# Kernel tuning notes

Measured on AMD Instinct MI355X. Metric: run time of the kernel, lower is better.

Reference implementation:

```python
import jax, jax.numpy as jnp
import numpy as np

B, H, W_, D, K = 64, 28, 28, 512, 32


def setup_inputs() -> dict:
    key = jax.random.key(0)
    k1, k2, k3 = jax.random.split(key, 3)
    x = jax.random.normal(k1, (B, H, W_, D), dtype=jnp.float32)
    # 1x1 conv weight, no bias: [D_in, K] (he_normal-like scale)
    W = jax.random.normal(k2, (D, K), dtype=jnp.float32) * np.sqrt(2.0 / D)
    # cluster offset tensor C (original shape (1,1,1,512,32), squeezed to [D,K])
    C = jax.random.normal(k3, (D, K), dtype=jnp.float32) * np.sqrt(2.0 / D)
    return {"x": x, "W": W, "C": C}


def reference(x, W, C):
    # 1x1 conv == per-pixel matmul: [B,H,W,D] @ [D,K] -> [B,H,W,K]
    s = jnp.einsum('bhwd,dk->bhwk', x, W)
    a = jax.nn.softmax(s, axis=-1)  # soft cluster assignment
    # Original math: v[b,d,k] = sum_{h,w} a[b,h,w,k] * (x[b,h,w,d] + C[d,k])
    # Algebraically identical split avoids the [B,H,W,D,K] 5D intermediate:
    #   sum_hw a*x  (matmul of assignments with features)
    # + (sum_hw a) * C  (cheap correction term)
    v = jnp.einsum('bhwk,bhwd->bdk', a, x) + jnp.sum(a, axis=(1, 2))[:, None, :] * C[None]
    return v.reshape(v.shape[0], -1)  # flatten -> [B, D*K]
```

## Files before the change

### kernel.cpp

```cpp
#include <hip/hip_runtime.h>

#define NB 64
#define HW 784
#define DD 512
#define KK 32
#define BPB 28
#define PPB 28
#define SLOTS 32

typedef __attribute__((ext_vector_type(8))) short bf16x8;
typedef __attribute__((ext_vector_type(4))) float f32x4;
typedef __attribute__((ext_vector_type(4))) unsigned short u16x4;

#define NBLK (NB * BPB)
#define PART_BYTES ((size_t)NBLK * 4 * 16 * 64 * 8)
#define WS_NEED    (PART_BYTES + (size_t)NBLK * KK * 4)

__device__ __forceinline__ unsigned short f2bf(float f) {
    unsigned u = __float_as_uint(f);
    u += 0x7fffu + ((u >> 16) & 1u);
    return (unsigned short)(u >> 16);
}
__device__ __forceinline__ float bf2f(unsigned short u) {
    return __uint_as_float((unsigned)u << 16);
}
__device__ __forceinline__ unsigned cvtpk(float a, float b) {
    unsigned r;
    asm("v_cvt_pk_bf16_f32 %0, %1, %2" : "=v"(r) : "v"(a), "v"(b));
    return r;
}

template <bool USE_WS>
__global__ __launch_bounds__(256) void netvlad_stage1(
    const float* __restrict__ x, const float* __restrict__ Wg,
    const float* __restrict__ Cg, float* __restrict__ out,
    void* __restrict__ ws)
{
    __shared__ __align__(16) unsigned short xs[28 * 520];
    __shared__ unsigned short spart[4][SLOTS][33];
    __shared__ __align__(16) unsigned short aTe[KK * 40];
    __shared__ float asumF[KK];

    const int tid = threadIdx.x;
    const int l   = tid & 63, w = tid >> 6;
    const int l15 = l & 15,  lq = l >> 4;
    const int k   = tid & 31, pg = tid >> 5;
    const int bid = blockIdx.x;
    const int b   = bid / BPB;
    const int pb  = (bid % BPB) * PPB;
    const float* xb = x + (size_t)b * HW * DD;

    {
        unsigned* sz = (unsigned*)spart;
#pragma unroll
        for (int i = 0; i < 8; ++i) sz[tid + 256*i] = 0u;
        if (tid < 2112 - 2048) sz[2048 + tid] = 0u;
    }

    bf16x8 Wf[4][2];
#pragma unroll
    for (int ks = 0; ks < 4; ++ks)
#pragma unroll
        for (int nt = 0; nt < 2; ++nt)
#pragma unroll
            for (int j = 0; j < 8; ++j)
                Wf[ks][nt][j] = (short)f2bf(Wg[(w*128 + ks*32 + lq*8 + j) * KK + nt*16 + l15]);

    f32x4 acc[2][8];
#pragma unroll
    for (int mt = 0; mt < 2; ++mt)
#pragma unroll
        for (int nt = 0; nt < 8; ++nt)
#pragma unroll
            for (int jj = 0; jj < 4; ++jj) acc[mt][nt][jj] = 0.f;
    float asum_part = 0.f;

#pragma unroll
    for (int h = 0; h < 2; ++h) {
        float4 r[7];
#pragma unroll
        for (int j = 0; j < 7; ++j) {
            const int f = tid + 256*(h*7 + j), row = f >> 7, c4 = f & 127;
            r[j] = *(const float4*)(xb + (size_t)(pb + row) * DD + c4*4);
        }
#pragma unroll
        for (int j = 0; j < 7; ++j) {
            const int f = tid + 256*(h*7 + j), row = f >> 7, c4 = f & 127;
            uint2 pk = make_uint2(cvtpk(r[j].x, r[j].y), cvtpk(r[j].z, r[j].w));
            *(uint2*)&xs[row*520 + c4*4] = pk;
        }
    }
    __syncthreads();

    {
        f32x4 sp[2][2];
#pragma unroll
        for (int mt = 0; mt < 2; ++mt)
#pragma unroll
            for (int nt = 0; nt < 2; ++nt)
#pragma unroll
                for (int jj = 0; jj < 4; ++jj) sp[mt][nt][jj] = 0.f;
#pragma unroll
        for (int ks = 0; ks < 4; ++ks) {
            bf16x8 af[2];
#pragma unroll
            for (int mt = 0; mt < 2; ++mt)
                af[mt] = *(const bf16x8*)&xs[(mt*16 + l15)*520 + w*128 + ks*32 + lq*8];
#pragma unroll
            for (int mt = 0; mt < 2; ++mt)
#pragma unroll
                for (int nt = 0; nt < 2; ++nt)
                    sp[mt][nt] = __builtin_amdgcn_mfma_f32_16x16x32_bf16(
                        af[mt], Wf[ks][nt], sp[mt][nt], 0, 0, 0);
        }
        const bool padrow = (lq == 3);
#pragma unroll
        for (int mt = 0; mt < 2; ++mt)
#pragma unroll
            for (int nt = 0; nt < 2; ++nt)
#pragma unroll
                for (int jj = 0; jj < 4; ++jj) {
                    unsigned short v = f2bf(sp[mt][nt][jj]);
                    if (mt == 1 && padrow) v = 0;
                    spart[w][mt*16 + lq*4 + jj][nt*16 + l15] = v;
                }
    }
    __syncthreads();

#pragma unroll
    for (int i = 0; i < 4; ++i) {
        const int p = pg + 8*i;
        const float s = bf2f(spart[0][p][k]) + bf2f(spart[1][p][k])
                      + bf2f(spart[2][p][k]) + bf2f(spart[3][p][k]);
        const float e = __expf(s);
        float su = e;
#pragma unroll
        for (int msk = 16; msk >= 1; msk >>= 1)
            su += __shfl_xor(su, msk);
        const float a = (p < PPB) ? e * __builtin_amdgcn_rcpf(su) : 0.f;
        asum_part += a;
        aTe[k*40 + p] = f2bf(a);
    }
    __syncthreads();

    {
        bf16x8 afr[2];
#pragma unroll
        for (int mt = 0; mt < 2; ++mt)
            afr[mt] = *(const bf16x8*)&aTe[(mt*16 + l15)*40 + lq*8];
#pragma unroll
        for (int nt = 0; nt < 8; ++nt) {
            const int d = w*128 + nt*16 + l15;
            bf16x8 bfr;
#pragma unroll
            for (int j = 0; j < 8; ++j) {
                const int jj = (j + 2*lq) & 7;
                bfr[jj] = (short)xs[(lq*8 + jj)*520 + d];
            }
#pragma unroll
            for (int mt = 0; mt < 2; ++mt)
                acc[mt][nt] = __builtin_amdgcn_mfma_f32_16x16x32_bf16(
                    afr[mt], bfr, acc[mt][nt], 0, 0, 0);
        }
    }
    __syncthreads();

    float* ared = (float*)aTe;
    ared[pg*KK + k] = asum_part;
    __syncthreads();
    float* wsA = (float*)((char*)ws + PART_BYTES);
    if (tid < KK) {
        float s = 0.f;
#pragma unroll
        for (int g = 0; g < 8; ++g) s += ared[g*KK + tid];
        if (USE_WS) wsA[(size_t)bid * KK + tid] = s;
        else        asumF[tid] = s;
    }

    if (USE_WS) {
        u16x4* o = (u16x4*)ws + ((size_t)bid * 4 + w) * (16 * 64);
#pragma unroll
        for (int mt = 0; mt < 2; ++mt)
#pragma unroll
            for (int nt = 0; nt < 8; ++nt) {
                uint2 pk = make_uint2(cvtpk(acc[mt][nt][0], acc[mt][nt][1]),
                                      cvtpk(acc[mt][nt][2], acc[mt][nt][3]));
                *(uint2*)&o[(mt*8 + nt)*64 + l] = pk;
            }
    } else {
        __syncthreads();
        float* ob = out + (size_t)b * (DD * KK);
#pragma unroll
        for (int mt = 0; mt < 2; ++mt)
#pragma unroll
            for (int nt = 0; nt < 8; ++nt)
#pragma unroll
                for (int jj = 0; jj < 4; ++jj) {
                    const int kk = mt*16 + lq*4 + jj;
                    const int d  = w*128 + nt*16 + l15;
                    atomicAdd(&ob[d*KK + kk], acc[mt][nt][jj] + asumF[kk] * Cg[d*KK + kk]);
                }
    }
}

__global__ __launch_bounds__(256) void netvlad_stage2(
    const void* __restrict__ ws, const float* __restrict__ Cg,
    float* __restrict__ out)
{
    __shared__ float lds[128 * 33];
    __shared__ float asumT[KK];

    const int t = threadIdx.x;
    const int b = blockIdx.x >> 2;
    const int jsl = blockIdx.x & 3;

    const float* wsA = (const float*)((const char*)ws + PART_BYTES);
    if (t < KK) {
        float s = 0.f;
#pragma unroll
        for (int p = 0; p < BPB; ++p)
            s += wsA[(size_t)(b*BPB + p) * KK + t];
        asumT[t] = s;
    }

    const u16x4* wsp = (const u16x4*)ws;
    float4 v[4];
#pragma unroll
    for (int i = 0; i < 4; ++i) v[i] = make_float4(0.f, 0.f, 0.f, 0.f);
    for (int p = 0; p < BPB; ++p) {
        const size_t base = ((size_t)(b*BPB + p) * 4 + jsl) * (16 * 64);
#pragma unroll
        for (int i = 0; i < 4; ++i) {
            const u16x4 u = wsp[base + t + 256*i];
            v[i].x += bf2f(u[0]); v[i].y += bf2f(u[1]);
            v[i].z += bf2f(u[2]); v[i].w += bf2f(u[3]);
        }
    }
#pragma unroll
    for (int i = 0; i < 4; ++i) {
        const int flat = t + 256*i;
        const int fr = flat >> 6, lane = flat & 63;
        const int mt = fr >> 3, nt = fr & 7;
        const int q = lane >> 4, r15 = lane & 15;
        const int dl = nt*16 + r15;
        const int kb = mt*16 + q*4;
        lds[dl*33 + kb + 0] = v[i].x;
        lds[dl*33 + kb + 1] = v[i].y;
        lds[dl*33 + kb + 2] = v[i].z;
        lds[dl*33 + kb + 3] = v[i].w;
    }
    __syncthreads();

    float* outw = out + (size_t)b * (DD*KK) + jsl * 128 * KK;
    const float* Cw = Cg + jsl * 128 * KK;
#pragma unroll
    for (int i = 0; i < 4; ++i) {
        const int o4 = t + 256*i;
        const int dl = o4 >> 3, kq = (o4 & 7) * 4;
        const float4 c4 = *(const float4*)&Cw[dl*KK + kq];
        float4 rr;
        rr.x = lds[dl*33 + kq + 0] + asumT[kq + 0] * c4.x;
        rr.y = lds[dl*33 + kq + 1] + asumT[kq + 1] * c4.y;
        rr.z = lds[dl*33 + kq + 2] + asumT[kq + 2] * c4.z;
        rr.w = lds[dl*33 + kq + 3] + asumT[kq + 3] * c4.w;
        ((float4*)outw)[o4] = rr;
    }
}

extern "C" void kernel_launch(void* const* d_in, const int* in_sizes, int n_in,
                              void* d_out, int out_size, void* d_ws, size_t ws_size,
                              hipStream_t stream) {
    const float* x = (const float*)d_in[0];
    const float* W = (const float*)d_in[1];
    const float* C = (const float*)d_in[2];
    float* out = (float*)d_out;

    if (ws_size >= WS_NEED) {
        netvlad_stage1<true><<<dim3(NBLK), dim3(256), 0, stream>>>(x, W, C, out, d_ws);
        netvlad_stage2<<<dim3(NB * 4), dim3(256), 0, stream>>>(d_ws, C, out);
    } else {
        hipMemsetAsync(out, 0, (size_t)out_size * sizeof(float), stream);
        netvlad_stage1<false><<<dim3(NBLK), dim3(256), 0, stream>>>(x, W, C, out, d_ws);
    }
}
```

Before: 48.63 us.

## Use 512-thread blocks in stage1, splitting MFMA work across eight waves

Doubles the stage-1 block size from 4 to 8 wavefronts. In the score GEMM each wave now covers one 16-row M-tile, and in the aggregation GEMM each wave covers 64 of the D columns instead of 128. The workspace partial layout changes to match, and stage 2 is reindexed to read it. The aim is more latency hiding and fewer accumulator registers per wave, at the cost of more barrier participants and duplicated W-fragment loads per block.

```diff
diff --git a/kernel.cpp b/kernel.cpp
--- a/kernel.cpp
+++ b/kernel.cpp
@@ -13,7 +13,7 @@
 typedef __attribute__((ext_vector_type(4))) unsigned short u16x4;
 
 #define NBLK (NB * BPB)
-#define PART_BYTES ((size_t)NBLK * 4 * 16 * 64 * 8)
+#define PART_BYTES ((size_t)NBLK * 8 * 8 * 64 * 8)
 #define WS_NEED    (PART_BYTES + (size_t)NBLK * KK * 4)
 
 __device__ __forceinline__ unsigned short f2bf(float f) {
@@ -31,7 +31,7 @@
 }
 
 template <bool USE_WS>
-__global__ __launch_bounds__(256) void netvlad_stage1(
+__global__ __launch_bounds__(512) void netvlad_stage1(
     const float* __restrict__ x, const float* __restrict__ Wg,
     const float* __restrict__ Cg, float* __restrict__ out,
     void* __restrict__ ws)
@@ -44,6 +44,8 @@
     const int tid = threadIdx.x;
     const int l   = tid & 63, w = tid >> 6;
     const int l15 = l & 15,  lq = l >> 4;
+    const int d4  = w & 3;
+    const int mtw = w >> 2;
     const int k   = tid & 31, pg = tid >> 5;
     const int bid = blockIdx.x;
     const int b   = bid / BPB;
@@ -53,7 +55,7 @@
     {
         unsigned* sz = (unsigned*)spart;
 #pragma unroll
-        for (int i = 0; i < 8; ++i) sz[tid + 256*i] = 0u;
+        for (int i = 0; i < 4; ++i) sz[tid + 512*i] = 0u;
         if (tid < 2112 - 2048) sz[2048 + tid] = 0u;
     }
 
@@ -64,28 +66,27 @@
         for (int nt = 0; nt < 2; ++nt)
 #pragma unroll
             for (int j = 0; j < 8; ++j)
-                Wf[ks][nt][j] = (short)f2bf(Wg[(w*128 + ks*32 + lq*8 + j) * KK + nt*16 + l15]);
-
-    f32x4 acc[2][8];
+                Wf[ks][nt][j] = (short)f2bf(Wg[(d4*128 + ks*32 + lq*8 + j) * KK + nt*16 + l15]);
+
+    f32x4 acc[2][4];
 #pragma unroll
     for (int mt = 0; mt < 2; ++mt)
 #pragma unroll
-        for (int nt = 0; nt < 8; ++nt)
+        for (int nt = 0; nt < 4; ++nt)
 #pragma unroll
             for (int jj = 0; jj < 4; ++jj) acc[mt][nt][jj] = 0.f;
     float asum_part = 0.f;
 
-#pragma unroll
-    for (int h = 0; h < 2; ++h) {
+    {
         float4 r[7];
 #pragma unroll
         for (int j = 0; j < 7; ++j) {
-            const int f = tid + 256*(h*7 + j), row = f >> 7, c4 = f & 127;
+            const int f = tid + 512*j, row = f >> 7, c4 = f & 127;
             r[j] = *(const float4*)(xb + (size_t)(pb + row) * DD + c4*4);
         }
 #pragma unroll
         for (int j = 0; j < 7; ++j) {
-            const int f = tid + 256*(h*7 + j), row = f >> 7, c4 = f & 127;
+            const int f = tid + 512*j, row = f >> 7, c4 = f & 127;
             uint2 pk = make_uint2(cvtpk(r[j].x, r[j].y), cvtpk(r[j].z, r[j].w));
             *(uint2*)&xs[row*520 + c4*4] = pk;
         }
@@ -93,43 +94,33 @@
     __syncthreads();
 
     {
-        f32x4 sp[2][2];
-#pragma unroll
-        for (int mt = 0; mt < 2; ++mt)
+        f32x4 sp[2];
+#pragma unroll
+        for (int nt = 0; nt < 2; ++nt)
+#pragma unroll
+            for (int jj = 0; jj < 4; ++jj) sp[nt][jj] = 0.f;
+#pragma unroll
+        for (int ks = 0; ks < 4; ++ks) {
+            const bf16x8 af = *(const bf16x8*)&xs[(mtw*16 + l15)*520 + d4*128 + ks*32 + lq*8];
 #pragma unroll
             for (int nt = 0; nt < 2; ++nt)
-#pragma unroll
-                for (int jj = 0; jj < 4; ++jj) sp[mt][nt][jj] = 0.f;
-#pragma unroll
-        for (int ks = 0; ks < 4; ++ks) {
-            bf16x8 af[2];
-#pragma unroll
-            for (int mt = 0; mt < 2; ++mt)
-                af[mt] = *(const bf16x8*)&xs[(mt*16 + l15)*520 + w*128 + ks*32 + lq*8];
-#pragma unroll
-            for (int mt = 0; mt < 2; ++mt)
-#pragma unroll
-                for (int nt = 0; nt < 2; ++nt)
-                    sp[mt][nt] = __builtin_amdgcn_mfma_f32_16x16x32_bf16(
-                        af[mt], Wf[ks][nt], sp[mt][nt], 0, 0, 0);
-        }
-        const bool padrow = (lq == 3);
-#pragma unroll
-        for (int mt = 0; mt < 2; ++mt)
-#pragma unroll
-            for (int nt = 0; nt < 2; ++nt)
-#pragma unroll
-                for (int jj = 0; jj < 4; ++jj) {
-                    unsigned short v = f2bf(sp[mt][nt][jj]);
-                    if (mt == 1 && padrow) v = 0;
-                    spart[w][mt*16 + lq*4 + jj][nt*16 + l15] = v;
-                }
-    }
-    __syncthreads();
-
-#pragma unroll
-    for (int i = 0; i < 4; ++i) {
-        const int p = pg + 8*i;
+                sp[nt] = __builtin_amdgcn_mfma_f32_16x16x32_bf16(
+                    af, Wf[ks][nt], sp[nt], 0, 0, 0);
+        }
+#pragma unroll
+        for (int nt = 0; nt < 2; ++nt)
+#pragma unroll
+            for (int jj = 0; jj < 4; ++jj) {
+                unsigned short v = f2bf(sp[nt][jj]);
+                if (mtw == 1 && lq == 3) v = 0;
+                spart[d4][mtw*16 + lq*4 + jj][nt*16 + l15] = v;
+            }
+    }
+    __syncthreads();
+
+#pragma unroll
+    for (int i = 0; i < 2; ++i) {
+        const int p = pg + 16*i;
         const float s = bf2f(spart[0][p][k]) + bf2f(spart[1][p][k])
                       + bf2f(spart[2][p][k]) + bf2f(spart[3][p][k]);
         const float e = __expf(s);
@@ -149,8 +140,8 @@
         for (int mt = 0; mt < 2; ++mt)
             afr[mt] = *(const bf16x8*)&aTe[(mt*16 + l15)*40 + lq*8];
 #pragma unroll
-        for (int nt = 0; nt < 8; ++nt) {
-            const int d = w*128 + nt*16 + l15;
+        for (int nt = 0; nt < 4; ++nt) {
+            const int d = w*64 + nt*16 + l15;
             bf16x8 bfr;
 #pragma unroll
             for (int j = 0; j < 8; ++j) {
@@ -172,20 +163,20 @@
     if (tid < KK) {
         float s = 0.f;
 #pragma unroll
-        for (int g = 0; g < 8; ++g) s += ared[g*KK + tid];
+        for (int g = 0; g < 16; ++g) s += ared[g*KK + tid];
         if (USE_WS) wsA[(size_t)bid * KK + tid] = s;
         else        asumF[tid] = s;
     }
 
     if (USE_WS) {
-        u16x4* o = (u16x4*)ws + ((size_t)bid * 4 + w) * (16 * 64);
+        u16x4* o = (u16x4*)ws + ((size_t)bid * 8 + w) * (8 * 64);
 #pragma unroll
         for (int mt = 0; mt < 2; ++mt)
 #pragma unroll
-            for (int nt = 0; nt < 8; ++nt) {
+            for (int nt = 0; nt < 4; ++nt) {
                 uint2 pk = make_uint2(cvtpk(acc[mt][nt][0], acc[mt][nt][1]),
                                       cvtpk(acc[mt][nt][2], acc[mt][nt][3]));
-                *(uint2*)&o[(mt*8 + nt)*64 + l] = pk;
+                *(uint2*)&o[(mt*4 + nt)*64 + l] = pk;
             }
     } else {
         __syncthreads();
@@ -193,11 +184,11 @@
 #pragma unroll
         for (int mt = 0; mt < 2; ++mt)
 #pragma unroll
-            for (int nt = 0; nt < 8; ++nt)
+            for (int nt = 0; nt < 4; ++nt)
 #pragma unroll
                 for (int jj = 0; jj < 4; ++jj) {
                     const int kk = mt*16 + lq*4 + jj;
-                    const int d  = w*128 + nt*16 + l15;
+                    const int d  = w*64 + nt*16 + l15;
                     atomicAdd(&ob[d*KK + kk], acc[mt][nt][jj] + asumF[kk] * Cg[d*KK + kk]);
                 }
     }
@@ -228,10 +219,13 @@
 #pragma unroll
     for (int i = 0; i < 4; ++i) v[i] = make_float4(0.f, 0.f, 0.f, 0.f);
     for (int p = 0; p < BPB; ++p) {
-        const size_t base = ((size_t)(b*BPB + p) * 4 + jsl) * (16 * 64);
+        const size_t base = (size_t)(b*BPB + p) * 8 * (8 * 64);
 #pragma unroll
         for (int i = 0; i < 4; ++i) {
-            const u16x4 u = wsp[base + t + 256*i];
+            const int flat = t + 256*i;
+            const int g = flat >> 6, lane = flat & 63;
+            const int w2 = g >> 3, fr = g & 7;
+            const u16x4 u = wsp[base + ((size_t)(2*jsl + w2) * 8 + fr)*64 + lane];
             v[i].x += bf2f(u[0]); v[i].y += bf2f(u[1]);
             v[i].z += bf2f(u[2]); v[i].w += bf2f(u[3]);
         }
@@ -239,10 +233,11 @@
 #pragma unroll
     for (int i = 0; i < 4; ++i) {
         const int flat = t + 256*i;
-        const int fr = flat >> 6, lane = flat & 63;
-        const int mt = fr >> 3, nt = fr & 7;
+        const int g = flat >> 6, lane = flat & 63;
+        const int w2 = g >> 3, fr = g & 7;
+        const int mt = fr >> 2, nt = fr & 3;
         const int q = lane >> 4, r15 = lane & 15;
-        const int dl = nt*16 + r15;
+        const int dl = w2*64 + nt*16 + r15;
         const int kb = mt*16 + q*4;
         lds[dl*33 + kb + 0] = v[i].x;
         lds[dl*33 + kb + 1] = v[i].y;
@@ -276,10 +271,10 @@
     float* out = (float*)d_out;
 
     if (ws_size >= WS_NEED) {
-        netvlad_stage1<true><<<dim3(NBLK), dim3(256), 0, stream>>>(x, W, C, out, d_ws);
+        netvlad_stage1<true><<<dim3(NBLK), dim3(512), 0, stream>>>(x, W, C, out, d_ws);
         netvlad_stage2<<<dim3(NB * 4), dim3(256), 0, stream>>>(d_ws, C, out);
     } else {
         hipMemsetAsync(out, 0, (size_t)out_size * sizeof(float), stream);
-        netvlad_stage1<false><<<dim3(NBLK), dim3(256), 0, stream>>>(x, W, C, out, d_ws);
-    }
-}
+        netvlad_stage1<false><<<dim3(NBLK), dim3(512), 0, stream>>>(x, W, C, out, d_ws);
+    }
+}
```

Result: slower. 50.75 us (+4.4%).
